# Kernel tuning notes

Hardware: AMD Instinct MI355X
Metric: run time of the kernel (lower is better)

Reference implementation:

```python
import jax, jax.numpy as jnp
import numpy as np
from math import factorial

# ---- config (matches init_kwargs) ----
N = 50000                 # batch of nodes/edges
LS = [0, 1, 2]            # l of each irrep block (in1, in2, out all share this)
MUL1, MUL2, MULO = 128, 1, 128
DIM = sum(2 * l + 1 for l in LS)  # 9 basis functions
INSTR = [(0,0,0),(0,1,1),(0,2,2),(1,0,1),(1,1,0),(1,1,1),(1,1,2),(1,2,1),(1,2,2),
         (2,0,2),(2,1,1),(2,1,2),(2,2,0),(2,2,1),(2,2,2)]
PATH_NUMEL = MUL1 * MUL2 * MULO   # uvw path shape
WEIGHT_NUMEL = len(INSTR) * PATH_NUMEL

# ---- Wigner 3j (real basis, e3nn convention) computed once in numpy ----

def _su2_cg(j1, m1, j2, m2, j3, m3):
    if m3 != m1 + m2:
        return 0.0
    vmin = int(max(-j1 + j2 + m3, -j1 + m1, 0))
    vmax = int(min(j2 + j3 + m1, j3 - j1 + j2, j3 + m3))
    f = lambda n: factorial(int(round(n)))
    C = ((2*j3+1) * f(j3+j1-j2) * f(j3-j1+j2) * f(j1+j2-j3) / f(j1+j2+j3+1)
         * f(j3+m3) * f(j3-m3) / (f(j1-m1)*f(j1+m1)*f(j2-m2)*f(j2+m2))) ** 0.5
    S = 0.0
    for v in range(vmin, vmax + 1):
        S += (-1.0)**(v + j2 + m2) / f(v) * f(j2+j3+m1-v) * f(j1-m1+v) / (
            f(j3-j1+j2-v) * f(j3+m3-v) * f(v+j1-j2-m3))
    return C * S

def _su2_clebsch_gordan(j1, j2, j3):
    mat = np.zeros((2*j1+1, 2*j2+1, 2*j3+1))
    for i, m1 in enumerate(range(-j1, j1+1)):
        for j, m2 in enumerate(range(-j2, j2+1)):
            for k, m3 in enumerate(range(-j3, j3+1)):
                mat[i, j, k] = _su2_cg(j1, m1, j2, m2, j3, m3)
    return mat

def _change_basis_real_to_complex(l):
    q = np.zeros((2*l+1, 2*l+1), dtype=np.complex128)
    for m in range(-l, 0):
        q[l+m, l+abs(m)] = 1/np.sqrt(2)
        q[l+m, l-abs(m)] = -1j/np.sqrt(2)
    q[l, l] = 1.0
    for m in range(1, l+1):
        q[l+m, l+abs(m)] = (-1)**m/np.sqrt(2)
        q[l+m, l-abs(m)] = 1j*(-1)**m/np.sqrt(2)
    return (-1j)**l * q

def wigner_3j(l1, l2, l3):
    C = _su2_clebsch_gordan(l1, l2, l3).astype(np.complex128)
    Q1 = _change_basis_real_to_complex(l1)
    Q2 = _change_basis_real_to_complex(l2)
    Q3 = _change_basis_real_to_complex(l3)
    C = np.einsum('ij,kl,mn,ikn->jlm', Q1, Q2, np.conj(Q3.T), C)
    assert np.abs(C.imag).max() < 1e-9
    C = C.real
    return C / np.linalg.norm(C)

_W3J = {}
for (i1, i2, io) in INSTR:
    key = (LS[i1], LS[i2], LS[io])
    if key not in _W3J:
        _W3J[key] = wigner_3j(*key).astype(np.float32)

# ---- normalization coefficients (irrep_normalization='component',
#      path_normalization='element', path_weight=1, path_weight_sqrt) ----
_ALPHA = []
for (i1, i2, io) in INSTR:
    x = sum(MUL1 * MUL2 for (_, _, c) in INSTR if c == io)  # num_elements per out
    _ALPHA.append(float(np.sqrt((2 * LS[io] + 1) / x)))

# per-l slices into the basis dim
_SLICES = []
_i = 0
for l in LS:
    _SLICES.append(slice(_i, _i + 2*l + 1))
    _i += 2*l + 1


def _forward(x1, x2, weight):
    # x1: (N, 9, MUL1) channel-last; x2: (N, 9, MUL2); weight: (WEIGHT_NUMEL,)
    x1_list = [x1[:, s, :] for s in _SLICES]
    x2_list = [x2[:, s, :] for s in _SLICES]
    outs = [[] for _ in LS]
    fw = 0
    for (i1, i2, io), alpha in zip(INSTR, _ALPHA):
        w = weight[fw:fw + PATH_NUMEL].reshape(MUL1, MUL2, MULO)[:, 0, :]  # squeeze v=1
        fw += PATH_NUMEL
        w3j = jnp.asarray(_W3J[(LS[i1], LS[i2], LS[io])], dtype=x1.dtype)
        # uvw branch: xx = einsum('ziu,zjv,ijk->zku'), then matmul with (u, w_out)
        xx = jnp.einsum('ziu,zjv,ijk->zku', x1_list[i1], x2_list[i2], w3j)
        outs[io].append(alpha * jnp.matmul(xx, w))  # (N, 2*l_out+1, MULO)
    summed = [o[0] if len(o) == 1 else sum(o[1:], o[0]) for o in outs]
    return jnp.concatenate(summed, axis=1)  # (N, 9, MULO)


def setup_inputs() -> dict:
    key = jax.random.key(0)
    k1, k2, k3 = jax.random.split(key, 3)
    return {
        'x1': jax.random.normal(k1, (N, DIM, MUL1), jnp.float32),
        'x2': jax.random.normal(k2, (N, DIM, MUL2), jnp.float32),
        'weight': jax.random.normal(k3, (WEIGHT_NUMEL,), jnp.float32),
    }


def reference(x1, x2, weight):
    return _forward(x1, x2, weight)
```

## Files before the change

### kernel.cpp

```cpp
#include <hip/hip_runtime.h>
#include <cmath>
#include <complex>
#include <vector>
#include <algorithm>

#define DEVFN __device__ __forceinline__

typedef short short8 __attribute__((ext_vector_type(8)));
typedef float f32x4  __attribute__((ext_vector_type(4)));

namespace {

constexpr int NNODE  = 50000;
constexpr int TILE_Z = 16;
constexpr int NBLOCK = NNODE / TILE_Z;
static_assert(NBLOCK * TILE_Z == NNODE, "tile");

constexpr int I_L1[15] = {0,0,0,1,1,1,1,1,1,2,2,2,2,2,2};
constexpr int I_L2[15] = {0,1,2,0,1,1,1,2,2,0,1,1,2,2,2};
constexpr int I_LO[15] = {0,1,2,1,0,1,2,1,2,2,1,2,0,1,2};
constexpr int W3OFF[15] = {0,1,10,35,44,53,80,125,170,245,270,315,390,415,490};
constexpr int LOFF[3] = {0,1,4};

struct TPParams { float w3j[615]; };
struct AlphaArg { float a[15]; };

double ffact(int n){ double r=1.0; for(int i=2;i<=n;++i) r*=i; return r; }

double su2cg(int j1,int m1,int j2,int m2,int j3,int m3){
  if(m3 != m1+m2) return 0.0;
  int vmin = std::max(std::max(-j1+j2+m3, -j1+m1), 0);
  int vmax = std::min(std::min(j2+j3+m1, j3-j1+j2), j3+m3);
  double C = std::sqrt((2.0*j3+1.0)*ffact(j3+j1-j2)*ffact(j3-j1+j2)*ffact(j1+j2-j3)
             /ffact(j1+j2+j3+1)
             *ffact(j3+m3)*ffact(j3-m3)
             /(ffact(j1-m1)*ffact(j1+m1)*ffact(j2-m2)*ffact(j2+m2)));
  double S = 0.0;
  for(int v=vmin; v<=vmax; ++v){
    double t = ffact(j2+j3+m1-v)*ffact(j1-m1+v)
             /(ffact(v)*ffact(j3-j1+j2-v)*ffact(j3+m3-v)*ffact(v+j1-j2-m3));
    S += ((v+j2+m2)&1) ? -t : t;
  }
  return C*S;
}

void cbasis(int l, std::complex<double>* q){
  int n = 2*l+1;
  for(int i=0;i<n*n;++i) q[i] = std::complex<double>(0.0,0.0);
  const double is2 = 1.0/std::sqrt(2.0);
  for(int m=-l; m<0; ++m){
    q[(l+m)*n + (l-m)] = std::complex<double>(is2, 0.0);
    q[(l+m)*n + (l+m)] = std::complex<double>(0.0, -is2);
  }
  q[l*n+l] = std::complex<double>(1.0, 0.0);
  for(int m=1; m<=l; ++m){
    double s = (m&1) ? -1.0 : 1.0;
    q[(l+m)*n + (l+m)] = std::complex<double>(s*is2, 0.0);
    q[(l+m)*n + (l-m)] = std::complex<double>(0.0, s*is2);
  }
  std::complex<double> ph;
  switch(l&3){ case 0: ph = std::complex<double>(1,0);  break;
               case 1: ph = std::complex<double>(0,-1); break;
               case 2: ph = std::complex<double>(-1,0); break;
               default: ph = std::complex<double>(0,1);  break; }
  for(int i=0;i<n*n;++i) q[i] *= ph;
}

void wigner3j_tab(int l1,int l2,int l3, float* dst){
  int n1=2*l1+1, n2=2*l2+1, n3=2*l3+1;
  std::vector<double> C(n1*n2*n3);
  for(int i=0;i<n1;++i) for(int k=0;k<n2;++k) for(int n=0;n<n3;++n)
    C[(i*n2+k)*n3+n] = su2cg(l1,i-l1, l2,k-l2, l3,n-l3);
  std::vector<std::complex<double>> Q1(n1*n1), Q2(n2*n2), Q3(n3*n3);
  cbasis(l1,Q1.data()); cbasis(l2,Q2.data()); cbasis(l3,Q3.data());
  std::vector<double> R(n1*n2*n3, 0.0);
  for(int j=0;j<n1;++j) for(int l=0;l<n2;++l) for(int m=0;m<n3;++m){
    std::complex<double> s(0,0);
    for(int i=0;i<n1;++i) for(int k=0;k<n2;++k) for(int n=0;n<n3;++n)
      s += Q1[i*n1+j]*Q2[k*n2+l]*std::conj(Q3[n*n3+m])*C[(i*n2+k)*n3+n];
    R[(j*n2+l)*n3+m] = s.real();
  }
  double nrm=0; for(double v:R) nrm += v*v; nrm = std::sqrt(nrm);
  for(int t=0;t<n1*n2*n3;++t) dst[t] = (float)(R[t]/nrm);
}

void fill_params(TPParams& P, AlphaArg& A){
  for(int ins=0; ins<15; ++ins)
    wigner3j_tab(I_L1[ins], I_L2[ins], I_LO[ins], P.w3j + W3OFF[ins]);
  int cnt[3] = {0,0,0};
  for(int ins=0; ins<15; ++ins) cnt[I_LO[ins]]++;
  for(int ins=0; ins<15; ++ins){
    int lo = I_LO[ins];
    A.a[ins] = (float)std::sqrt((2.0*lo+1.0)/(128.0*cnt[lo]));
  }
}

}

DEVFN unsigned f2bf(float f){
  unsigned u = __float_as_uint(f);
  return (u + 0x7fffu + ((u>>16)&1u)) >> 16;
}
DEVFN unsigned pkbf(float a, float b){ return f2bf(a) | (f2bf(b)<<16); }

template<typename T, typename F>
DEVFN T bc(F f){ static_assert(sizeof(T)==sizeof(F), "size"); T t; __builtin_memcpy(&t,&f,sizeof(T)); return t; }

__global__ __launch_bounds__(256)
void prep_kernel(const float* __restrict__ w, unsigned short* __restrict__ ws,
                 AlphaArg al)
{
  int t = blockIdx.x*256 + threadIdx.x;
  int p = t >> 14, rem = t & 16383, u = rem >> 7, col = rem & 127;
  float v = w[t] * al.a[p];
  int gs = (u>>3) ^ (col & 15);
  ws[(p<<14) + (col<<7) + (gs<<3) + (u&7)] = (unsigned short)f2bf(v);
}

template<int INS>
DEVFN void path_phaseA(const TPParams& P, const unsigned x1p[9][4],
                       const float x2r[9], uint4* sxxU4, int z, int ug)
{
  constexpr int L1 = I_L1[INS], L2 = I_L2[INS], LO = I_LO[INS];
  constexpr int N1 = 2*L1+1, N2 = 2*L2+1, NO = 2*LO+1;
  constexpr int O1 = LOFF[L1], O2 = LOFF[L2], W3 = W3OFF[INS];

  float cc[NO][N1];
  #pragma unroll
  for(int k=0;k<NO;++k){
    #pragma unroll
    for(int i=0;i<N1;++i){
      float s = 0.f;
      #pragma unroll
      for(int j=0;j<N2;++j)
        s += P.w3j[W3 + (i*N2+j)*NO + k] * x2r[O2 + j];
      cc[k][i] = s;
    }
  }
  float a8[NO][8];
  #pragma unroll
  for(int k=0;k<NO;++k){
    #pragma unroll
    for(int e=0;e<8;++e) a8[k][e]=0.f;
  }
  #pragma unroll
  for(int i=0;i<N1;++i){
    float xf[8];
    #pragma unroll
    for(int pr=0;pr<4;++pr){
      unsigned u = x1p[O1+i][pr];
      xf[2*pr]   = __uint_as_float(u << 16);
      xf[2*pr+1] = __uint_as_float(u & 0xffff0000u);
    }
    #pragma unroll
    for(int k=0;k<NO;++k){
      #pragma unroll
      for(int e=0;e<8;++e) a8[k][e] += cc[k][i]*xf[e];
    }
  }
  #pragma unroll
  for(int k=0;k<NO;++k){
    uint4 o;
    o.x = pkbf(a8[k][0], a8[k][1]);
    o.y = pkbf(a8[k][2], a8[k][3]);
    o.z = pkbf(a8[k][4], a8[k][5]);
    o.w = pkbf(a8[k][6], a8[k][7]);
    sxxU4[(k*16 + z)*16 + ((ug ^ z) & 15)] = o;
  }
}

template<int INS>
DEVFN void path_gemm(const uint4* sxxU4, const uint4* sWTU4,
                     f32x4 acc[9][2], int lane, int wv)
{
  constexpr int LO = I_LO[INS], NO = 2*LO+1, OO = LOFF[LO];
  const int m = lane & 15, q = lane >> 4;
  #pragma unroll
  for(int ks=0; ks<4; ++ks){
    const int g  = ks*4 + q;
    const int gp = (g ^ m) & 15;
    short8 a[NO];
    #pragma unroll
    for(int k=0;k<NO;++k)
      a[k] = bc<short8>(sxxU4[(k*16 + m)*16 + gp]);
    #pragma unroll
    for(int ct=0; ct<2; ++ct){
      const int w = (wv*2 + ct)*16 + m;
      short8 b = bc<short8>(sWTU4[w*16 + gp]);
      #pragma unroll
      for(int k=0;k<NO;++k)
        acc[OO+k][ct] = __builtin_amdgcn_mfma_f32_16x16x32_bf16(a[k], b, acc[OO+k][ct], 0,0,0);
    }
  }
}

DEVFN void stage_wt(const uint4* __restrict__ wsrc, uint4* sWT, int tid){
  #pragma unroll
  for(int r=0;r<8;++r){
    uint4 v = wsrc[r*256 + tid];
    sWT[r*256 + tid] = v;
  }
}

__global__ __launch_bounds__(256, 2)
void tp_kernel(const float* __restrict__ x1, const float* __restrict__ x2,
               const unsigned short* __restrict__ wsb, float* __restrict__ out,
               TPParams P)
{
  __shared__ uint4 sxxU4[5*16*16];
  __shared__ uint4 sWTU4[2048];

  const int tid = threadIdx.x;
  const long zbase = (long)blockIdx.x * TILE_Z;
  const int z = tid >> 4, ug = tid & 15;
  const int lane = tid & 63, wv = tid >> 6;

  unsigned x1p[9][4];
  float x2r[9];
  {
    const float* xsrc = x1 + (zbase + z)*1152 + ug*8;
    #pragma unroll
    for(int i=0;i<9;++i){
      float4 a = *reinterpret_cast<const float4*>(xsrc + i*128);
      float4 b = *reinterpret_cast<const float4*>(xsrc + i*128 + 4);
      x1p[i][0] = pkbf(a.x, a.y); x1p[i][1] = pkbf(a.z, a.w);
      x1p[i][2] = pkbf(b.x, b.y); x1p[i][3] = pkbf(b.z, b.w);
    }
    #pragma unroll
    for(int j=0;j<9;++j) x2r[j] = x2[(zbase + z)*9 + j];
  }

  f32x4 acc[9][2];
  #pragma unroll
  for(int t=0;t<9;++t){
    #pragma unroll
    for(int c=0;c<2;++c){ f32x4 zz = {0.f,0.f,0.f,0.f}; acc[t][c] = zz; }
  }

  const uint4* wsbU4 = reinterpret_cast<const uint4*>(wsb);

#define DO_PATH(n)                                               \
  stage_wt(wsbU4 + (n)*2048, sWTU4, tid);                        \
  path_phaseA<n>(P, x1p, x2r, sxxU4, z, ug);                     \
  __syncthreads();                                               \
  path_gemm<n>(sxxU4, sWTU4, acc, lane, wv);                     \
  __syncthreads();

  DO_PATH(0)  DO_PATH(1)  DO_PATH(2)  DO_PATH(3)  DO_PATH(4)
  DO_PATH(5)  DO_PATH(6)  DO_PATH(7)  DO_PATH(8)  DO_PATH(9)
  DO_PATH(10) DO_PATH(11) DO_PATH(12) DO_PATH(13) DO_PATH(14)
#undef DO_PATH

  const int col = lane & 15, q = lane >> 4;
  #pragma unroll
  for(int t=0;t<9;++t){
    #pragma unroll
    for(int ct=0;ct<2;++ct){
      #pragma unroll
      for(int r=0;r<4;++r)
        out[(zbase + q*4 + r)*1152 + t*128 + (wv*2 + ct)*16 + col] = acc[t][ct][r];
    }
  }
}

extern "C" void kernel_launch(void* const* d_in, const int* in_sizes, int n_in,
                              void* d_out, int out_size, void* d_ws, size_t ws_size,
                              hipStream_t stream)
{
  (void)in_sizes; (void)n_in; (void)out_size; (void)ws_size;
  const float* x1 = (const float*)d_in[0];
  const float* x2 = (const float*)d_in[1];
  const float* wt = (const float*)d_in[2];
  float* out = (float*)d_out;
  unsigned short* wsb = (unsigned short*)d_ws;

  TPParams P; AlphaArg A;
  fill_params(P, A);

  prep_kernel<<<dim3(960), dim3(256), 0, stream>>>(wt, wsb, A);
  tp_kernel<<<dim3(NBLOCK), dim3(256), 0, stream>>>(x1, x2, wsb, out, P);
}
```

Measured before the change: 501.4 us.

## Group paths by output l to shrink accumulators, use direct global-to-LDS loads

```diff
diff --git a/kernel.cpp b/kernel.cpp
--- a/kernel.cpp
+++ b/kernel.cpp
@@ -171,9 +171,9 @@
 
 template<int INS>
 DEVFN void path_gemm(const uint4* sxxU4, const uint4* sWTU4,
-                     f32x4 acc[9][2], int lane, int wv)
-{
-  constexpr int LO = I_LO[INS], NO = 2*LO+1, OO = LOFF[LO];
+                     f32x4 (*acc)[2], int lane, int wv)
+{
+  constexpr int LO = I_LO[INS], NO = 2*LO+1;
   const int m = lane & 15, q = lane >> 4;
   #pragma unroll
   for(int ks=0; ks<4; ++ks){
@@ -189,20 +189,40 @@
       short8 b = bc<short8>(sWTU4[w*16 + gp]);
       #pragma unroll
       for(int k=0;k<NO;++k)
-        acc[OO+k][ct] = __builtin_amdgcn_mfma_f32_16x16x32_bf16(a[k], b, acc[OO+k][ct], 0,0,0);
+        acc[k][ct] = __builtin_amdgcn_mfma_f32_16x16x32_bf16(a[k], b, acc[k][ct], 0,0,0);
     }
   }
 }
 
 DEVFN void stage_wt(const uint4* __restrict__ wsrc, uint4* sWT, int tid){
+  typedef __attribute__((address_space(1))) const void gvoid;
+  typedef __attribute__((address_space(3))) void lvoid;
   #pragma unroll
   for(int r=0;r<8;++r){
-    uint4 v = wsrc[r*256 + tid];
-    sWT[r*256 + tid] = v;
-  }
-}
-
-__global__ __launch_bounds__(256, 2)
+    gvoid* gp = (gvoid*)(wsrc + r*256 + tid);
+    lvoid* lp = (lvoid*)(sWT  + r*256 + tid);
+    __builtin_amdgcn_global_load_lds(gp, lp, 16, 0, 0);
+  }
+}
+
+template<int LO, int NO>
+DEVFN void write_out(float* __restrict__ out, long zbase,
+                     const f32x4 (*acc)[2], int lane, int wv)
+{
+  constexpr int OO = LOFF[LO];
+  const int col = lane & 15, q = lane >> 4;
+  #pragma unroll
+  for(int k=0;k<NO;++k){
+    #pragma unroll
+    for(int ct=0;ct<2;++ct){
+      #pragma unroll
+      for(int r=0;r<4;++r)
+        out[(zbase + q*4 + r)*1152 + (OO+k)*128 + (wv*2 + ct)*16 + col] = acc[k][ct][r];
+    }
+  }
+}
+
+__global__ __launch_bounds__(256, 3)
 void tp_kernel(const float* __restrict__ x1, const float* __restrict__ x2,
                const unsigned short* __restrict__ wsb, float* __restrict__ out,
                TPParams P)
@@ -230,37 +250,57 @@
     for(int j=0;j<9;++j) x2r[j] = x2[(zbase + z)*9 + j];
   }
 
-  f32x4 acc[9][2];
-  #pragma unroll
-  for(int t=0;t<9;++t){
-    #pragma unroll
-    for(int c=0;c<2;++c){ f32x4 zz = {0.f,0.f,0.f,0.f}; acc[t][c] = zz; }
-  }
-
   const uint4* wsbU4 = reinterpret_cast<const uint4*>(wsb);
 
-#define DO_PATH(n)                                               \
+#define DO_PATH(n, ACC)                                          \
   stage_wt(wsbU4 + (n)*2048, sWTU4, tid);                        \
   path_phaseA<n>(P, x1p, x2r, sxxU4, z, ug);                     \
   __syncthreads();                                               \
-  path_gemm<n>(sxxU4, sWTU4, acc, lane, wv);                     \
+  path_gemm<n>(sxxU4, sWTU4, ACC, lane, wv);                     \
   __syncthreads();
 
-  DO_PATH(0)  DO_PATH(1)  DO_PATH(2)  DO_PATH(3)  DO_PATH(4)
-  DO_PATH(5)  DO_PATH(6)  DO_PATH(7)  DO_PATH(8)  DO_PATH(9)
-  DO_PATH(10) DO_PATH(11) DO_PATH(12) DO_PATH(13) DO_PATH(14)
+  {
+    f32x4 a0[1][2];
+    #pragma unroll
+    for(int c=0;c<2;++c){ f32x4 zz = {0.f,0.f,0.f,0.f}; a0[0][c] = zz; }
+    DO_PATH(0,  a0)
+    DO_PATH(4,  a0)
+    DO_PATH(12, a0)
+    write_out<0,1>(out, zbase, a0, lane, wv);
+  }
+
+  {
+    f32x4 a1[3][2];
+    #pragma unroll
+    for(int k=0;k<3;++k){
+      #pragma unroll
+      for(int c=0;c<2;++c){ f32x4 zz = {0.f,0.f,0.f,0.f}; a1[k][c] = zz; }
+    }
+    DO_PATH(1,  a1)
+    DO_PATH(3,  a1)
+    DO_PATH(5,  a1)
+    DO_PATH(7,  a1)
+    DO_PATH(10, a1)
+    DO_PATH(13, a1)
+    write_out<1,3>(out, zbase, a1, lane, wv);
+  }
+
+  {
+    f32x4 a2[5][2];
+    #pragma unroll
+    for(int k=0;k<5;++k){
+      #pragma unroll
+      for(int c=0;c<2;++c){ f32x4 zz = {0.f,0.f,0.f,0.f}; a2[k][c] = zz; }
+    }
+    DO_PATH(2,  a2)
+    DO_PATH(6,  a2)
+    DO_PATH(8,  a2)
+    DO_PATH(9,  a2)
+    DO_PATH(11, a2)
+    DO_PATH(14, a2)
+    write_out<2,5>(out, zbase, a2, lane, wv);
+  }
 #undef DO_PATH
-
-  const int col = lane & 15, q = lane >> 4;
-  #pragma unroll
-  for(int t=0;t<9;++t){
-    #pragma unroll
-    for(int ct=0;ct<2;++ct){
-      #pragma unroll
-      for(int r=0;r<4;++r)
-        out[(zbase + q*4 + r)*1152 + t*128 + (wv*2 + ct)*16 + col] = acc[t][ct][r];
-    }
-  }
 }
 
 extern "C" void kernel_launch(void* const* d_in, const int* in_sizes, int n_in,
@@ -274,8 +314,10 @@
   float* out = (float*)d_out;
   unsigned short* wsb = (unsigned short*)d_ws;
 
-  TPParams P; AlphaArg A;
-  fill_params(P, A);
+  static TPParams P;
+  static AlphaArg A;
+  static bool inited = false;
+  if(!inited){ fill_params(P, A); inited = true; }
 
   prep_kernel<<<dim3(960), dim3(256), 0, stream>>>(wt, wsb, A);
   tp_kernel<<<dim3(NBLOCK), dim3(256), 0, stream>>>(x1, x2, wsb, out, P);
```

Result: no change. 507.6 us (+1.2%).

## Prefetch weight fragments into registers and group paths by output irrep

Applied to the files above, without the earlier changes.

```diff
diff --git a/kernel.cpp b/kernel.cpp
--- a/kernel.cpp
+++ b/kernel.cpp
@@ -103,6 +103,12 @@
 }
 DEVFN unsigned pkbf(float a, float b){ return f2bf(a) | (f2bf(b)<<16); }
 
+DEVFN unsigned cvtpk(float a, float b){
+  unsigned r;
+  asm("v_cvt_pk_bf16_f32 %0, %1, %2" : "=v"(r) : "v"(a), "v"(b));
+  return r;
+}
+
 template<typename T, typename F>
 DEVFN T bc(F f){ static_assert(sizeof(T)==sizeof(F), "size"); T t; __builtin_memcpy(&t,&f,sizeof(T)); return t; }
 
@@ -110,11 +116,24 @@
 void prep_kernel(const float* __restrict__ w, unsigned short* __restrict__ ws,
                  AlphaArg al)
 {
-  int t = blockIdx.x*256 + threadIdx.x;
-  int p = t >> 14, rem = t & 16383, u = rem >> 7, col = rem & 127;
-  float v = w[t] * al.a[p];
-  int gs = (u>>3) ^ (col & 15);
-  ws[(p<<14) + (col<<7) + (gs<<3) + (u&7)] = (unsigned short)f2bf(v);
+  int v = blockIdx.x*256 + threadIdx.x;
+  int p = v >> 11, r = v & 2047;
+  int ks = (r>>6)&3, ln = r&63;
+  int q = ln>>4, m = ln&15;
+  int wcol = (r>>8)*16 + m;
+  float a = al.a[p];
+  const float* src = w + p*16384 + wcol;
+  uint4 o;
+  unsigned tmp[4];
+  #pragma unroll
+  for(int pr=0; pr<4; ++pr){
+    int u0 = (ks*4+q)*8 + pr*2;
+    float lo = src[u0*128]     * a;
+    float hi = src[(u0+1)*128] * a;
+    tmp[pr] = pkbf(lo, hi);
+  }
+  o.x = tmp[0]; o.y = tmp[1]; o.z = tmp[2]; o.w = tmp[3];
+  reinterpret_cast<uint4*>(ws)[v] = o;
 }
 
 template<int INS>
@@ -161,44 +180,69 @@
   #pragma unroll
   for(int k=0;k<NO;++k){
     uint4 o;
-    o.x = pkbf(a8[k][0], a8[k][1]);
-    o.y = pkbf(a8[k][2], a8[k][3]);
-    o.z = pkbf(a8[k][4], a8[k][5]);
-    o.w = pkbf(a8[k][6], a8[k][7]);
+    o.x = cvtpk(a8[k][0], a8[k][1]);
+    o.y = cvtpk(a8[k][2], a8[k][3]);
+    o.z = cvtpk(a8[k][4], a8[k][5]);
+    o.w = cvtpk(a8[k][6], a8[k][7]);
     sxxU4[(k*16 + z)*16 + ((ug ^ z) & 15)] = o;
   }
 }
 
+DEVFN void loadB(const uint4* __restrict__ src, short8 (&bfr)[2][4],
+                 int lane, int wv){
+  #pragma unroll
+  for(int ct=0; ct<2; ++ct){
+    #pragma unroll
+    for(int ks=0; ks<4; ++ks)
+      bfr[ct][ks] = bc<short8>(src[(wv*2+ct)*256 + ks*64 + lane]);
+  }
+}
+
 template<int INS>
-DEVFN void path_gemm(const uint4* sxxU4, const uint4* sWTU4,
-                     f32x4 acc[9][2], int lane, int wv)
-{
-  constexpr int LO = I_LO[INS], NO = 2*LO+1, OO = LOFF[LO];
+DEVFN void path_gemm(const uint4* sxxU4, const short8 (&bfr)[2][4],
+                     f32x4 (*acc)[2], int lane)
+{
+  constexpr int NO = 2*I_LO[INS]+1;
   const int m = lane & 15, q = lane >> 4;
   #pragma unroll
   for(int ks=0; ks<4; ++ks){
-    const int g  = ks*4 + q;
-    const int gp = (g ^ m) & 15;
+    const int gp = ((ks*4 + q) ^ m) & 15;
     short8 a[NO];
     #pragma unroll
     for(int k=0;k<NO;++k)
       a[k] = bc<short8>(sxxU4[(k*16 + m)*16 + gp]);
     #pragma unroll
     for(int ct=0; ct<2; ++ct){
-      const int w = (wv*2 + ct)*16 + m;
-      short8 b = bc<short8>(sWTU4[w*16 + gp]);
       #pragma unroll
       for(int k=0;k<NO;++k)
-        acc[OO+k][ct] = __builtin_amdgcn_mfma_f32_16x16x32_bf16(a[k], b, acc[OO+k][ct], 0,0,0);
-    }
-  }
-}
-
-DEVFN void stage_wt(const uint4* __restrict__ wsrc, uint4* sWT, int tid){
-  #pragma unroll
-  for(int r=0;r<8;++r){
-    uint4 v = wsrc[r*256 + tid];
-    sWT[r*256 + tid] = v;
+        acc[k][ct] = __builtin_amdgcn_mfma_f32_16x16x32_bf16(a[k], bfr[ct][ks], acc[k][ct], 0,0,0);
+    }
+  }
+}
+
+template<int LO, int NO>
+DEVFN void write_out(float* __restrict__ out, long zbase,
+                     const f32x4 (*acc)[2], int lane, int wv)
+{
+  constexpr int OO = LOFF[LO];
+  const int col = lane & 15, q = lane >> 4;
+  #pragma unroll
+  for(int k=0;k<NO;++k){
+    #pragma unroll
+    for(int ct=0;ct<2;++ct){
+      #pragma unroll
+      for(int r=0;r<4;++r)
+        out[(zbase + q*4 + r)*1152 + (OO+k)*128 + (wv*2 + ct)*16 + col] = acc[k][ct][r];
+    }
+  }
+}
+
+template<int NK>
+DEVFN void zacc(f32x4 (*a)[2]){
+  #pragma unroll
+  for(int k=0;k<NK;++k){
+    #pragma unroll
+    for(int c=0;c<2;++c){ f32x4 zz = {0.f,0.f,0.f,0.f}; a[k][c] = zz; }
   }
 }
 
@@ -207,14 +251,19 @@
                const unsigned short* __restrict__ wsb, float* __restrict__ out,
                TPParams P)
 {
-  __shared__ uint4 sxxU4[5*16*16];
-  __shared__ uint4 sWTU4[2048];
+  __shared__ uint4 sxx[5*16*16];
 
   const int tid = threadIdx.x;
   const long zbase = (long)blockIdx.x * TILE_Z;
   const int z = tid >> 4, ug = tid & 15;
   const int lane = tid & 63, wv = tid >> 6;
 
+  const uint4* ws2U4 = reinterpret_cast<const uint4*>(wsb);
+
+  short8 B0[2][4], B1[2][4];
+
+  loadB(ws2U4 + 0*2048, B0, lane, wv);
+
   unsigned x1p[9][4];
   float x2r[9];
   {
@@ -223,44 +272,59 @@
     for(int i=0;i<9;++i){
       float4 a = *reinterpret_cast<const float4*>(xsrc + i*128);
       float4 b = *reinterpret_cast<const float4*>(xsrc + i*128 + 4);
-      x1p[i][0] = pkbf(a.x, a.y); x1p[i][1] = pkbf(a.z, a.w);
-      x1p[i][2] = pkbf(b.x, b.y); x1p[i][3] = pkbf(b.z, b.w);
+      x1p[i][0] = cvtpk(a.x, a.y); x1p[i][1] = cvtpk(a.z, a.w);
+      x1p[i][2] = cvtpk(b.x, b.y); x1p[i][3] = cvtpk(b.z, b.w);
     }
     #pragma unroll
     for(int j=0;j<9;++j) x2r[j] = x2[(zbase + z)*9 + j];
   }
 
-  f32x4 acc[9][2];
-  #pragma unroll
-  for(int t=0;t<9;++t){
-    #pragma unroll
-    for(int c=0;c<2;++c){ f32x4 zz = {0.f,0.f,0.f,0.f}; acc[t][c] = zz; }
-  }
-
-  const uint4* wsbU4 = reinterpret_cast<const uint4*>(wsb);
-
-#define DO_PATH(n)                                               \
-  stage_wt(wsbU4 + (n)*2048, sWTU4, tid);                        \
-  path_phaseA<n>(P, x1p, x2r, sxxU4, z, ug);                     \
-  __syncthreads();                                               \
-  path_gemm<n>(sxxU4, sWTU4, acc, lane, wv);                     \
-  __syncthreads();
-
-  DO_PATH(0)  DO_PATH(1)  DO_PATH(2)  DO_PATH(3)  DO_PATH(4)
-  DO_PATH(5)  DO_PATH(6)  DO_PATH(7)  DO_PATH(8)  DO_PATH(9)
-  DO_PATH(10) DO_PATH(11) DO_PATH(12) DO_PATH(13) DO_PATH(14)
-#undef DO_PATH
-
-  const int col = lane & 15, q = lane >> 4;
-  #pragma unroll
-  for(int t=0;t<9;++t){
-    #pragma unroll
-    for(int ct=0;ct<2;++ct){
-      #pragma unroll
-      for(int r=0;r<4;++r)
-        out[(zbase + q*4 + r)*1152 + t*128 + (wv*2 + ct)*16 + col] = acc[t][ct][r];
-    }
-  }
+  path_phaseA<0>(P, x1p, x2r, sxx, z, ug);
+
+#define BAR_LGKM                                             \
+  asm volatile("s_waitcnt lgkmcnt(0)" ::: "memory");         \
+  __builtin_amdgcn_s_barrier();
+
+  BAR_LGKM
+
+#define STEP(CUR, NXT, ACC, BCUR, BNXT)                      \
+  loadB(ws2U4 + (NXT)*2048, BNXT, lane, wv);                 \
+  path_gemm<CUR>(sxx, BCUR, ACC, lane);                      \
+  BAR_LGKM                                                   \
+  path_phaseA<NXT>(P, x1p, x2r, sxx, z, ug);                 \
+  BAR_LGKM
+
+#define STEP_LAST(CUR, ACC, BCUR)                            \
+  path_gemm<CUR>(sxx, BCUR, ACC, lane);
+
+  f32x4 a0[1][2], a1[3][2], a2[5][2];
+
+  zacc<1>(a0); zacc<3>(a1); zacc<5>(a2);
+
+  STEP(0,  4,  a0, B0, B1)
+  STEP(4,  12, a0, B1, B0)
+  STEP(12, 1,  a0, B0, B1)
+  write_out<0,1>(out, zbase, a0, lane, wv);
+
+  STEP(1,  3,  a1, B1, B0)
+  STEP(3,  5,  a1, B0, B1)
+  STEP(5,  7,  a1, B1, B0)
+  STEP(7,  10, a1, B0, B1)
+  STEP(10, 13, a1, B1, B0)
+  STEP(13, 2,  a1, B0, B1)
+  write_out<1,3>(out, zbase, a1, lane, wv);
+
+  STEP(2,  6,  a2, B1, B0)
+  STEP(6,  8,  a2, B0, B1)
+  STEP(8,  9,  a2, B1, B0)
+  STEP(9,  11, a2, B0, B1)
+  STEP(11, 14, a2, B1, B0)
+  STEP_LAST(14, a2, B0)
+  write_out<2,5>(out, zbase, a2, lane, wv);
+
+#undef STEP
+#undef STEP_LAST
+#undef BAR_LGKM
 }
 
 extern "C" void kernel_launch(void* const* d_in, const int* in_sizes, int n_in,
@@ -274,9 +338,11 @@
   float* out = (float*)d_out;
   unsigned short* wsb = (unsigned short*)d_ws;
 
-  TPParams P; AlphaArg A;
-  fill_params(P, A);
-
-  prep_kernel<<<dim3(960), dim3(256), 0, stream>>>(wt, wsb, A);
+  static TPParams P;
+  static AlphaArg A;
+  static bool inited = false;
+  if(!inited){ fill_params(P, A); inited = true; }
+
+  prep_kernel<<<dim3(120), dim3(256), 0, stream>>>(wt, wsb, A);
   tp_kernel<<<dim3(NBLOCK), dim3(256), 0, stream>>>(x1, x2, wsb, out, P);
 }
```

Result: faster. 455.6 us (-9.1%).
